# Kernel tuning notes

Hardware: AMD Instinct MI355X
Metric: run time of the kernel (lower is better)

The kernel has to match this reference:

```python
import jax, jax.numpy as jnp
import numpy as np

N_NODES = 50000
N_EDGES = 800000
IN_DIM = 162
HID = 256  # layer_1_feats == layer_2_feats (required by the stack op)


def _lin(k, fan_in, fan_out):
    kw, kb = jax.random.split(k)
    bound = 1.0 / np.sqrt(fan_in)
    w = jax.random.uniform(kw, (fan_in, fan_out), jnp.float32, -bound, bound)
    b = jax.random.uniform(kb, (fan_out,), jnp.float32, -bound, bound)
    return w, b


def setup_inputs() -> dict:
    key = jax.random.key(0)
    ks = jax.random.split(key, 12)
    feat = jax.random.normal(ks[0], (N_NODES, IN_DIM), jnp.float32)
    edge_index = jax.random.randint(ks[1], (2, N_EDGES), 0, N_NODES, jnp.int64)
    g0_w, g0_b = _lin(ks[2], IN_DIM, HID)
    g1_w, g1_b = _lin(ks[3], HID, HID)
    g2_w, g2_b = _lin(ks[4], HID, HID)
    gl_w, gl_b = _lin(ks[5], HID, HID)
    m1a_w, m1a_b = _lin(ks[6], IN_DIM, HID)
    m1b_w, m1b_b = _lin(ks[7], HID, HID)
    m2a_w, m2a_b = _lin(ks[8], HID, HID)
    m2b_w, m2b_b = _lin(ks[9], HID, HID)
    return dict(feat=feat, edge_index=edge_index,
                g0_w=g0_w, g0_b=g0_b, g1_w=g1_w, g1_b=g1_b,
                g2_w=g2_w, g2_b=g2_b, gl_w=gl_w, gl_b=gl_b,
                m1a_w=m1a_w, m1a_b=m1a_b, m1b_w=m1b_w, m1b_b=m1b_b,
                m2a_w=m2a_w, m2a_b=m2a_b, m2b_w=m2b_w, m2b_b=m2b_b)


def _gin_conv(x, src, dst, wa, ba, wb, bb):
    # DGL GINConv('sum'), eps=0: h = MLP(x + sum_{u->v} x[u])
    agg = jax.ops.segment_sum(x[src], dst, num_segments=N_NODES)
    h = jax.nn.relu((x + agg) @ wa + ba)
    return jax.nn.relu(h @ wb + bb)


def reference(feat, edge_index, g0_w, g0_b, g1_w, g1_b, g2_w, g2_b,
              gl_w, gl_b, m1a_w, m1a_b, m1b_w, m1b_b, m2a_w, m2a_b,
              m2b_w, m2b_b):
    src, dst = edge_index[0], edge_index[1]
    # layer-0 graph embedding from raw features
    g_emb0 = jax.nn.relu(jnp.sum(feat, 0) @ g0_w + g0_b)
    # GIN layer 1
    node1 = _gin_conv(feat, src, dst, m1a_w, m1a_b, m1b_w, m1b_b)
    g_emb1 = jax.nn.relu(jnp.sum(node1, 0) @ g1_w + g1_b)
    # GIN layer 2
    node2 = _gin_conv(node1, src, dst, m2a_w, m2a_b, m2b_w, m2b_b)
    g_emb2 = jax.nn.relu(jnp.sum(node2, 0) @ g2_w + g2_b)
    # sum of per-layer graph embeddings -> last linear
    g_sum = g_emb0 + g_emb1 + g_emb2
    g_last = jax.nn.relu(g_sum @ gl_w + gl_b)
    return node2 + g_last  # broadcast [N, HID] + [HID]
```

## Files before the change

kernel.cpp:

```cpp
#include <hip/hip_runtime.h>

#define N_NODES 50000
#define N_EDGES 800000
#define IN_DIM  162
#define HID     256
#define KPAD1   192
#define NB      ((N_NODES + 255) / 256)

typedef __bf16 bf16;
typedef __bf16 bf16x8 __attribute__((ext_vector_type(8)));
typedef __bf16 bf16x4 __attribute__((ext_vector_type(4)));
typedef float  f32x4  __attribute__((ext_vector_type(4)));
typedef float  f32x8  __attribute__((ext_vector_type(8)));
typedef float  f32x16 __attribute__((ext_vector_type(16)));

__device__ __forceinline__ void wf_one(const float* W, bf16* Wf, int K, int E)
{
    int e    = E & 7;
    int lane = (E >> 3) & 63;
    int fb   = (E >> 9) & 15;
    int ks   = E >> 13;
    int n = (fb >> 1) * 32 + (lane & 31);
    int k = ks * 32 + (fb & 1) * 16 + (lane >> 5) * 8 + e;
    Wf[E] = (k < K) ? (bf16)W[(size_t)k * HID + n] : (bf16)0.0f;
}

__global__ void wt_fragmajor_all(const float* __restrict__ m1aw, const float* __restrict__ m1bw,
                                 const float* __restrict__ m2aw, const float* __restrict__ m2bw,
                                 bf16* __restrict__ Wf1, bf16* __restrict__ Wf2,
                                 bf16* __restrict__ Wf3, bf16* __restrict__ Wf4)
{
    const int R1 = HID * KPAD1;
    const int R2 = HID * HID;
    int idx = blockIdx.x * blockDim.x + threadIdx.x;
    if (idx < R1)                 wf_one(m1aw, Wf1, IN_DIM, idx);
    else if (idx < R1 + R2)       wf_one(m1bw, Wf2, HID, idx - R1);
    else if (idx < R1 + 2 * R2)   wf_one(m2aw, Wf3, HID, idx - R1 - R2);
    else if (idx < R1 + 3 * R2)   wf_one(m2bw, Wf4, HID, idx - R1 - 2 * R2);
}

__global__ void feat_to_bf16(const float* __restrict__ feat, bf16* __restrict__ featbf)
{
    int idx = blockIdx.x * blockDim.x + threadIdx.x;
    int r = idx / (KPAD1 / 4);
    int c4 = (idx - r * (KPAD1 / 4)) * 4;
    if (r >= N_NODES) return;
    bf16x4 o;
#pragma unroll
    for (int j = 0; j < 4; ++j) {
        int c = c4 + j;
        o[j] = (c < IN_DIM) ? (bf16)feat[(size_t)r * IN_DIM + c] : (bf16)0.0f;
    }
    int gch = c4 / 24;
    int off = c4 - gch * 24;
    *(bf16x4*)(featbf + ((size_t)gch * N_NODES + r) * 24 + off) = o;
}

__global__ void colsum_feat8(const float* __restrict__ feat, float* __restrict__ colsum8)
{
    int c  = threadIdx.x;
    int r0 = blockIdx.x * 50;
    if (c >= IN_DIM) return;
    float acc = 0.0f;
#pragma unroll 2
    for (int i = 0; i < 50; ++i) {
        int r = r0 + i;
        if (r < N_NODES) acc += feat[(size_t)r * IN_DIM + c];
    }
    atomicAdd(&colsum8[(blockIdx.x & 7) * KPAD1 + c], acc);
}

__global__ void degree_hist(const int* __restrict__ dst, int* __restrict__ deg)
{
    int e = blockIdx.x * blockDim.x + threadIdx.x;
    atomicAdd(&deg[dst[e]], 1);
}

__global__ void block_degsum(const int* __restrict__ deg, int* __restrict__ bsum)
{
    __shared__ int s[256];
    int t = threadIdx.x;
    int idx = blockIdx.x * 256 + t;
    int v = (idx < N_NODES) ? deg[idx] : 0;
    s[t] = v;
    __syncthreads();
    for (int off = 128; off > 0; off >>= 1) {
        if (t < off) s[t] += s[t + off];
        __syncthreads();
    }
    if (t == 0) bsum[blockIdx.x] = s[0];
}

__global__ void scan_bsum(const int* __restrict__ bsum, int* __restrict__ gsum)
{
    __shared__ int s[256];
    int t = threadIdx.x;
    int v = (t < NB) ? bsum[t] : 0;
    s[t] = v;
    __syncthreads();
    for (int off = 1; off < 256; off <<= 1) {
        int u = (t >= off) ? s[t - off] : 0;
        __syncthreads();
        s[t] += u;
        __syncthreads();
    }
    gsum[t] = s[t] - v;
}

__global__ void block_scan_write(const int* __restrict__ deg, const int* __restrict__ gsum,
                                 int* __restrict__ rowptr, int* __restrict__ cursor)
{
    __shared__ int s[256];
    int t = threadIdx.x;
    int idx = blockIdx.x * 256 + t;
    int v = (idx < N_NODES) ? deg[idx] : 0;
    s[t] = v;
    __syncthreads();
    for (int off = 1; off < 256; off <<= 1) {
        int u = (t >= off) ? s[t - off] : 0;
        __syncthreads();
        s[t] += u;
        __syncthreads();
    }
    int excl = s[t] - v + gsum[blockIdx.x];
    if (idx < N_NODES) {
        rowptr[idx] = excl;
        cursor[idx] = excl;
    }
    if (idx == 0) rowptr[N_NODES] = N_EDGES;
}

__global__ void csr_fill(const int* __restrict__ src, const int* __restrict__ dst,
                         int* __restrict__ cursor, int* __restrict__ csr_src)
{
    int e = blockIdx.x * blockDim.x + threadIdx.x;
    int p = atomicAdd(&cursor[dst[e]], 1);
    csr_src[p] = src[e];
}

template<int CHUNK, int NACT>
__launch_bounds__(256)
__global__ void gather_v5(const bf16* __restrict__ xin,
                          const int* __restrict__ rowptr,
                          const int* __restrict__ csr_src,
                          bf16* __restrict__ xout)
{
    const int g    = blockIdx.x & 7;
    const int tile = blockIdx.x >> 3;
    const int wv   = threadIdx.x >> 6;
    const int lane = threadIdx.x & 63;
    const int q    = lane >> 4;
    const int j    = lane & 15;
    const int e    = j >> 2;
    const int c4   = j & 3;
    const int n    = tile * 16 + wv * 4 + q;
    const bool valid = (n < N_NODES);
    const bool act   = (c4 < NACT);
    const int  ce    = c4 * 8;
    const bf16* base = xin + (size_t)g * N_NODES * CHUNK;

    int r0 = 0, deg = 0;
    if (valid) {
        r0  = rowptr[n];
        deg = rowptr[n + 1] - r0;
    }

    int a0 = r0 + j;        if (a0 > N_EDGES - 1) a0 = N_EDGES - 1;
    int a1 = r0 + 16 + j;   if (a1 > N_EDGES - 1) a1 = N_EDGES - 1;
    const int i0 = csr_src[a0];
    const int i1 = csr_src[a1];

    f32x8 acc;
#pragma unroll
    for (int t = 0; t < 8; ++t) acc[t] = 0.0f;
    if (valid && e == 0 && act) {
        bf16x8 t0 = *(const bf16x8*)(base + (size_t)n * CHUNK + ce);
#pragma unroll
        for (int t = 0; t < 8; ++t) acc[t] = (float)t0[t];
    }

    const int lb = lane & ~3;

    {
        const int s0 = __shfl(i0, lb + 0, 64);
        const int s1 = __shfl(i0, lb + 1, 64);
        const int s2 = __shfl(i0, lb + 2, 64);
        const int s3 = __shfl(i0, lb + 3, 64);
        const int p0 = 4 * e;
        if (act) {
            bf16x8 u0 = *(const bf16x8*)(base + (size_t)s0 * CHUNK + ce);
            bf16x8 u1 = *(const bf16x8*)(base + (size_t)s1 * CHUNK + ce);
            bf16x8 u2 = *(const bf16x8*)(base + (size_t)s2 * CHUNK + ce);
            bf16x8 u3 = *(const bf16x8*)(base + (size_t)s3 * CHUNK + ce);
            if (p0 + 0 < deg) {
#pragma unroll
                for (int t = 0; t < 8; ++t) acc[t] += (float)u0[t];
            }
            if (p0 + 1 < deg) {
#pragma unroll
                for (int t = 0; t < 8; ++t) acc[t] += (float)u1[t];
            }
            if (p0 + 2 < deg) {
#pragma unroll
                for (int t = 0; t < 8; ++t) acc[t] += (float)u2[t];
            }
            if (p0 + 3 < deg) {
#pragma unroll
                for (int t = 0; t < 8; ++t) acc[t] += (float)u3[t];
            }
        }
    }

    {
        const int s0 = __shfl(i1, lb + 0, 64);
        const int s1 = __shfl(i1, lb + 1, 64);
        const int s2 = __shfl(i1, lb + 2, 64);
        const int s3 = __shfl(i1, lb + 3, 64);
        const int p0 = 16 + 4 * e;
        if (act && p0 < deg) {
            bf16x8 u0 = *(const bf16x8*)(base + (size_t)s0 * CHUNK + ce);
            bf16x8 u1 = *(const bf16x8*)(base + (size_t)s1 * CHUNK + ce);
            bf16x8 u2 = *(const bf16x8*)(base + (size_t)s2 * CHUNK + ce);
            bf16x8 u3 = *(const bf16x8*)(base + (size_t)s3 * CHUNK + ce);
            {
#pragma unroll
                for (int t = 0; t < 8; ++t) acc[t] += (float)u0[t];
            }
            if (p0 + 1 < deg) {
#pragma unroll
                for (int t = 0; t < 8; ++t) acc[t] += (float)u1[t];
            }
            if (p0 + 2 < deg) {
#pragma unroll
                for (int t = 0; t < 8; ++t) acc[t] += (float)u2[t];
            }
            if (p0 + 3 < deg) {
#pragma unroll
                for (int t = 0; t < 8; ++t) acc[t] += (float)u3[t];
            }
        }
    }

    for (int p = 32 + e; p < deg; p += 4) {
        const int s = csr_src[r0 + p];
        if (act) {
            bf16x8 u = *(const bf16x8*)(base + (size_t)s * CHUNK + ce);
#pragma unroll
            for (int t = 0; t < 8; ++t) acc[t] += (float)u[t];
        }
    }

#pragma unroll
    for (int t = 0; t < 8; ++t) {
        acc[t] += __shfl_xor(acc[t], 4, 64);
        acc[t] += __shfl_xor(acc[t], 8, 64);
    }

    if (valid && e == 0 && act) {
        bf16x8 o;
#pragma unroll
        for (int t = 0; t < 8; ++t) o[t] = (bf16)acc[t];
        __builtin_nontemporal_store(o,
            (bf16x8*)(xout + ((size_t)g * N_NODES + n) * CHUNK + ce));
    }
}

template<int KPAD, int ACHUNK, int OCHUNK>
__launch_bounds__(512)
__global__ void gemm_mlp8(const bf16* __restrict__ X,
                          const bf16* __restrict__ Wf1,
                          const float* __restrict__ bias1,
                          const bf16* __restrict__ Wf2,
                          const float* __restrict__ bias2,
                          bf16* __restrict__ out_bf,
                          float* __restrict__ colsum,
                          int M)
{
    __shared__ __align__(128) bf16 sH[64 * HID];
    __shared__ float cs[HID];

    const int tid  = threadIdx.x;
    const int w    = tid >> 6;
    const int lane = tid & 63;
    const int p    = lane >> 5;
    const int cn   = lane & 31;
    const int rw   = w & 1;
    const int cw   = w >> 1;
    const int m_base = blockIdx.x * 64;

    int arow = m_base + rw * 32 + cn;
    if (arow >= M) arow = M - 1;

    f32x16 accA, accB;
#pragma unroll
    for (int r = 0; r < 16; ++r) { accA[r] = 0.0f; accB[r] = 0.0f; }

#pragma unroll
    for (int ks = 0; ks < KPAD / 32; ++ks) {
#pragma unroll
        for (int kk = 0; kk < 2; ++kk) {
            bf16x8 a;
            if constexpr (ACHUNK == 0) {
                a = *(const bf16x8*)(X + (size_t)arow * KPAD + ks * 32 + kk * 16 + p * 8);
            } else {
                const int e   = ks * 32 + kk * 16 + p * 8;
                const int gch = e / ACHUNK;
                const int off = e - gch * ACHUNK;
                a = *(const bf16x8*)(X + ((size_t)gch * N_NODES + arow) * ACHUNK + off);
            }
            const int jg0 = cw * 2;
            bf16x8 b0 = *(const bf16x8*)(Wf1 + (((ks * 16 + (jg0 + 0) * 2 + kk) * 64) + lane) * 8);
            bf16x8 b1 = *(const bf16x8*)(Wf1 + (((ks * 16 + (jg0 + 1) * 2 + kk) * 64) + lane) * 8);
            accA = __builtin_amdgcn_mfma_f32_32x32x16_bf16(a, b0, accA, 0, 0, 0);
            accB = __builtin_amdgcn_mfma_f32_32x32x16_bf16(a, b1, accB, 0, 0, 0);
        }
    }

    char* sHb = (char*)sH;
#pragma unroll
    for (int jj = 0; jj < 2; ++jj) {
        const int col = cw * 64 + jj * 32 + cn;
        const float bv = bias1[col];
#pragma unroll
        for (int r = 0; r < 16; ++r) {
            const int rowl = (r & 3) + 8 * (r >> 2) + 4 * p;
            const int rowf = rw * 32 + rowl;
            float v = (jj == 0 ? accA[r] : accB[r]) + bv;
            v = v > 0.0f ? v : 0.0f;
            int ba = rowf * (HID * 2) + col * 2;
            ba ^= (rowf & 31) << 4;
            *(bf16*)(sHb + ba) = (bf16)v;
        }
    }
    __syncthreads();

#pragma unroll
    for (int r = 0; r < 16; ++r) { accA[r] = 0.0f; accB[r] = 0.0f; }

    const int hrow = rw * 32 + cn;
    const int hswz = (hrow & 31) << 4;
#pragma unroll
    for (int ks = 0; ks < HID / 32; ++ks) {
#pragma unroll
        for (int kk = 0; kk < 2; ++kk) {
            const int kb = (ks * 32 + kk * 16 + p * 8) * 2;
            bf16x8 a = *(const bf16x8*)(sHb + ((hrow * (HID * 2) + kb) ^ hswz));
            const int jg0 = cw * 2;
            bf16x8 b0 = *(const bf16x8*)(Wf2 + (((ks * 16 + (jg0 + 0) * 2 + kk) * 64) + lane) * 8);
            bf16x8 b1 = *(const bf16x8*)(Wf2 + (((ks * 16 + (jg0 + 1) * 2 + kk) * 64) + lane) * 8);
            accA = __builtin_amdgcn_mfma_f32_32x32x16_bf16(a, b0, accA, 0, 0, 0);
            accB = __builtin_amdgcn_mfma_f32_32x32x16_bf16(a, b1, accB, 0, 0, 0);
        }
    }

    if (colsum) {
        if (tid < HID) cs[tid] = 0.0f;
        __syncthreads();
    }

#pragma unroll
    for (int jj = 0; jj < 2; ++jj) {
        const int jg  = cw * 2 + jj;
        const int col = jg * 32 + cn;
        const float bv = bias2[col];
        float part = 0.0f;
#pragma unroll
        for (int r = 0; r < 16; ++r) {
            int rl = (r & 3) + 8 * (r >> 2) + 4 * p;
            int mo = m_base + rw * 32 + rl;
            if (mo < M) {
                float v = (jj == 0 ? accA[r] : accB[r]) + bv;
                v = v > 0.0f ? v : 0.0f;
                if constexpr (OCHUNK == 0)
                    out_bf[(size_t)mo * HID + col] = (bf16)v;
                else
                    out_bf[((size_t)jg * N_NODES + mo) * OCHUNK + cn] = (bf16)v;
                part += v;
            }
        }
        if (colsum) {
            part += __shfl_xor(part, 32, 64);
            if (p == 0) atomicAdd(&cs[col], part);
        }
    }

    if (colsum) {
        __syncthreads();
        if (tid < HID) atomicAdd(&colsum[tid], cs[tid]);
    }
}

__global__ void graph_head(const float* __restrict__ cs0_8,
                           const float* __restrict__ cs1,
                           const float* __restrict__ cs2,
                           const float* __restrict__ g0w, const float* __restrict__ g0b,
                           const float* __restrict__ g1w, const float* __restrict__ g1b,
                           const float* __restrict__ g2w, const float* __restrict__ g2b,
                           const float* __restrict__ glw, const float* __restrict__ glb,
                           float* __restrict__ gvec)
{
    __shared__ float v0[IN_DIM], v1[HID], v2[HID], gs[HID];
    int t = threadIdx.x;
    if (t < IN_DIM) {
        float s = 0.0f;
#pragma unroll
        for (int i = 0; i < 8; ++i) s += cs0_8[i * KPAD1 + t];
        v0[t] = s;
    }
    v1[t] = cs1[t];
    v2[t] = cs2[t];
    __syncthreads();

    float a0 = 0.0f, a1 = 0.0f, a2 = 0.0f;
    for (int k = 0; k < IN_DIM; ++k) a0 += v0[k] * g0w[k * HID + t];
    for (int k = 0; k < HID; ++k) {
        a1 += v1[k] * g1w[k * HID + t];
        a2 += v2[k] * g2w[k * HID + t];
    }
    float e0 = fmaxf(a0 + g0b[t], 0.0f);
    float e1 = fmaxf(a1 + g1b[t], 0.0f);
    float e2 = fmaxf(a2 + g2b[t], 0.0f);
    gs[t] = e0 + e1 + e2;
    __syncthreads();

    float a3 = 0.0f;
    for (int k = 0; k < HID; ++k) a3 += gs[k] * glw[k * HID + t];
    gvec[t] = fmaxf(a3 + glb[t], 0.0f);
}

__global__ void final_add(const bf16* __restrict__ node2,
                          const float* __restrict__ gvec,
                          float* __restrict__ out)
{
    int idx = blockIdx.x * blockDim.x + threadIdx.x;
    size_t base = (size_t)idx * 4;
    int c = (int)(base & (HID - 1));
    bf16x4 v = *(const bf16x4*)(node2 + base);
    f32x4 g = *(const f32x4*)(gvec + c);
    f32x4 o;
#pragma unroll
    for (int j = 0; j < 4; ++j) o[j] = (float)v[j] + g[j];
    *(f32x4*)(out + base) = o;
}

extern "C" void kernel_launch(void* const* d_in, const int* in_sizes, int n_in,
                              void* d_out, int out_size, void* d_ws, size_t ws_size,
                              hipStream_t stream)
{
    const float* feat = (const float*)d_in[0];
    const int*   ei   = (const int*)d_in[1];
    const int*   src  = ei;
    const int*   dst  = ei + N_EDGES;
    const float* g0w = (const float*)d_in[2],  *g0b = (const float*)d_in[3];
    const float* g1w = (const float*)d_in[4],  *g1b = (const float*)d_in[5];
    const float* g2w = (const float*)d_in[6],  *g2b = (const float*)d_in[7];
    const float* glw = (const float*)d_in[8],  *glb = (const float*)d_in[9];
    const float* m1aw = (const float*)d_in[10], *m1ab = (const float*)d_in[11];
    const float* m1bw = (const float*)d_in[12], *m1bb = (const float*)d_in[13];
    const float* m2aw = (const float*)d_in[14], *m2ab = (const float*)d_in[15];
    const float* m2bw = (const float*)d_in[16], *m2bb = (const float*)d_in[17];
    float* out = (float*)d_out;

    char* ws = (char*)d_ws;
    size_t off = 0;
    auto alloc = [&](size_t bytes) -> void* {
        void* p = ws + off;
        off += (bytes + 255) & ~(size_t)255;
        return p;
    };
    bf16*  featbf = (bf16*)alloc((size_t)N_NODES * KPAD1 * 2);
    bf16*  xsum  = (bf16*) alloc((size_t)N_NODES * KPAD1 * 2);
    bf16*  y2    = (bf16*) alloc((size_t)N_NODES * HID * 2);
    bf16*  node2 = (bf16*) alloc((size_t)N_NODES * HID * 2);
    bf16*  node1 = (bf16*) alloc((size_t)N_NODES * HID * 2);
    bf16*  Wf1   = (bf16*) alloc((size_t)HID * KPAD1 * 2);
    bf16*  Wf2   = (bf16*) alloc((size_t)HID * HID * 2);
    bf16*  Wf3   = (bf16*) alloc((size_t)HID * HID * 2);
    bf16*  Wf4   = (bf16*) alloc((size_t)HID * HID * 2);
    int*   deg     = (int*)alloc((size_t)N_NODES * 4);
    int*   rowptr  = (int*)alloc((size_t)(N_NODES + 1) * 4);
    int*   cursor  = (int*)alloc((size_t)N_NODES * 4);
    int*   csr_src = (int*)alloc((size_t)N_EDGES * 4);
    int*   bsum    = (int*)alloc(256 * 4);
    int*   gsum    = (int*)alloc(256 * 4);
    float* csums   = (float*)alloc((8 * KPAD1 + 256 + 256 + 256) * 4);
    float* colsum0_8 = csums;
    float* colsum1   = csums + 8 * KPAD1;
    float* colsum2   = csums + 8 * KPAD1 + 256;
    float* gvec      = csums + 8 * KPAD1 + 512;

    hipMemsetAsync(csums, 0, (8 * KPAD1 + 512) * 4, stream);
    hipMemsetAsync(deg, 0, (size_t)N_NODES * 4, stream);

    wt_fragmajor_all<<<(HID * KPAD1 + 3 * HID * HID + 255) / 256, 256, 0, stream>>>(
        m1aw, m1bw, m2aw, m2bw, Wf1, Wf2, Wf3, Wf4);

    feat_to_bf16<<<((size_t)N_NODES * (KPAD1 / 4) + 255) / 256, 256, 0, stream>>>(feat, featbf);
    colsum_feat8<<<1000, 192, 0, stream>>>(feat, colsum0_8);

    degree_hist<<<N_EDGES / 256, 256, 0, stream>>>(dst, deg);
    block_degsum<<<NB, 256, 0, stream>>>(deg, bsum);
    scan_bsum<<<1, 256, 0, stream>>>(bsum, gsum);
    block_scan_write<<<NB, 256, 0, stream>>>(deg, gsum, rowptr, cursor);
    csr_fill<<<N_EDGES / 256, 256, 0, stream>>>(src, dst, cursor, csr_src);

    const int gtiles = (N_NODES + 15) / 16;
    gather_v5<24, 3><<<gtiles * 8, 256, 0, stream>>>(featbf, rowptr, csr_src, xsum);

    const int gblocks = (N_NODES + 63) / 64;
    gemm_mlp8<KPAD1, 24, 32><<<gblocks, 512, 0, stream>>>(
        xsum, Wf1, m1ab, Wf2, m1bb, node1, colsum1, N_NODES);
    gather_v5<32, 4><<<gtiles * 8, 256, 0, stream>>>(node1, rowptr, csr_src, y2);
    gemm_mlp8<HID, 32, 0><<<gblocks, 512, 0, stream>>>(
        y2, Wf3, m2ab, Wf4, m2bb, node2, colsum2, N_NODES);
    graph_head<<<1, 256, 0, stream>>>(colsum0_8, colsum1, colsum2,
                                      g0w, g0b, g1w, g1b, g2w, g2b, glw, glb, gvec);
    final_add<<<((size_t)N_NODES * HID / 4 + 255) / 256, 256, 0, stream>>>(node2, gvec, out);
    (void)in_sizes; (void)n_in; (void)out_size; (void)ws_size;
}
```

Measured before the change: 468.3 us.

## Fuse prep kernels into one launch and retile MLP GEMM to 4 waves

```diff
diff --git a/kernel.cpp b/kernel.cpp
--- a/kernel.cpp
+++ b/kernel.cpp
@@ -25,55 +25,66 @@
     Wf[E] = (k < K) ? (bf16)W[(size_t)k * HID + n] : (bf16)0.0f;
 }
 
-__global__ void wt_fragmajor_all(const float* __restrict__ m1aw, const float* __restrict__ m1bw,
-                                 const float* __restrict__ m2aw, const float* __restrict__ m2bw,
-                                 bf16* __restrict__ Wf1, bf16* __restrict__ Wf2,
-                                 bf16* __restrict__ Wf3, bf16* __restrict__ Wf4)
-{
-    const int R1 = HID * KPAD1;
-    const int R2 = HID * HID;
-    int idx = blockIdx.x * blockDim.x + threadIdx.x;
-    if (idx < R1)                 wf_one(m1aw, Wf1, IN_DIM, idx);
-    else if (idx < R1 + R2)       wf_one(m1bw, Wf2, HID, idx - R1);
-    else if (idx < R1 + 2 * R2)   wf_one(m2aw, Wf3, HID, idx - R1 - R2);
-    else if (idx < R1 + 3 * R2)   wf_one(m2bw, Wf4, HID, idx - R1 - 2 * R2);
-}
-
-__global__ void feat_to_bf16(const float* __restrict__ feat, bf16* __restrict__ featbf)
-{
-    int idx = blockIdx.x * blockDim.x + threadIdx.x;
-    int r = idx / (KPAD1 / 4);
-    int c4 = (idx - r * (KPAD1 / 4)) * 4;
-    if (r >= N_NODES) return;
-    bf16x4 o;
-#pragma unroll
-    for (int j = 0; j < 4; ++j) {
-        int c = c4 + j;
-        o[j] = (c < IN_DIM) ? (bf16)feat[(size_t)r * IN_DIM + c] : (bf16)0.0f;
-    }
-    int gch = c4 / 24;
-    int off = c4 - gch * 24;
-    *(bf16x4*)(featbf + ((size_t)gch * N_NODES + r) * 24 + off) = o;
-}
-
-__global__ void colsum_feat8(const float* __restrict__ feat, float* __restrict__ colsum8)
-{
-    int c  = threadIdx.x;
-    int r0 = blockIdx.x * 50;
-    if (c >= IN_DIM) return;
-    float acc = 0.0f;
+#define WTB  ((HID * KPAD1 + 3 * HID * HID + 255) / 256)
+#define FTB  (((size_t)N_NODES * (KPAD1 / 4) + 255) / 256)
+#define CSB  1000
+#define DGB  (N_EDGES / 256)
+
+__global__ void prep_all(const float* __restrict__ m1aw, const float* __restrict__ m1bw,
+                         const float* __restrict__ m2aw, const float* __restrict__ m2bw,
+                         bf16* __restrict__ Wf1, bf16* __restrict__ Wf2,
+                         bf16* __restrict__ Wf3, bf16* __restrict__ Wf4,
+                         const float* __restrict__ feat, bf16* __restrict__ featbf,
+                         float* __restrict__ colsum8,
+                         const int* __restrict__ dst, int* __restrict__ deg)
+{
+    const int b   = blockIdx.x;
+    const int tid = threadIdx.x;
+
+    if (b < WTB) {
+        const int R1 = HID * KPAD1;
+        const int R2 = HID * HID;
+        int idx = b * 256 + tid;
+        if (idx < R1)                 wf_one(m1aw, Wf1, IN_DIM, idx);
+        else if (idx < R1 + R2)       wf_one(m1bw, Wf2, HID, idx - R1);
+        else if (idx < R1 + 2 * R2)   wf_one(m2aw, Wf3, HID, idx - R1 - R2);
+        else if (idx < R1 + 3 * R2)   wf_one(m2bw, Wf4, HID, idx - R1 - 2 * R2);
+        return;
+    }
+    if (b < WTB + FTB) {
+        int idx = (b - WTB) * 256 + tid;
+        int r = idx / (KPAD1 / 4);
+        int c4 = (idx - r * (KPAD1 / 4)) * 4;
+        if (r >= N_NODES) return;
+        bf16x4 o;
+#pragma unroll
+        for (int j = 0; j < 4; ++j) {
+            int c = c4 + j;
+            o[j] = (c < IN_DIM) ? (bf16)feat[(size_t)r * IN_DIM + c] : (bf16)0.0f;
+        }
+        int gch = c4 / 24;
+        int off = c4 - gch * 24;
+        *(bf16x4*)(featbf + ((size_t)gch * N_NODES + r) * 24 + off) = o;
+        return;
+    }
+    if (b < WTB + FTB + CSB) {
+        int csb = b - WTB - FTB;
+        int c = tid;
+        int r0 = csb * 50;
+        if (c >= IN_DIM) return;
+        float acc = 0.0f;
 #pragma unroll 2
-    for (int i = 0; i < 50; ++i) {
-        int r = r0 + i;
-        if (r < N_NODES) acc += feat[(size_t)r * IN_DIM + c];
-    }
-    atomicAdd(&colsum8[(blockIdx.x & 7) * KPAD1 + c], acc);
-}
-
-__global__ void degree_hist(const int* __restrict__ dst, int* __restrict__ deg)
-{
-    int e = blockIdx.x * blockDim.x + threadIdx.x;
-    atomicAdd(&deg[dst[e]], 1);
+        for (int i = 0; i < 50; ++i) {
+            int r = r0 + i;
+            if (r < N_NODES) acc += feat[(size_t)r * IN_DIM + c];
+        }
+        atomicAdd(&colsum8[(csb & 7) * KPAD1 + c], acc);
+        return;
+    }
+    {
+        int e = (b - WTB - FTB - CSB) * 256 + tid;
+        atomicAdd(&deg[dst[e]], 1);
+    }
 }
 
 __global__ void block_degsum(const int* __restrict__ deg, int* __restrict__ bsum)
@@ -266,8 +277,8 @@
 }
 
 template<int KPAD, int ACHUNK, int OCHUNK>
-__launch_bounds__(512)
-__global__ void gemm_mlp8(const bf16* __restrict__ X,
+__launch_bounds__(256)
+__global__ void gemm_mlp4(const bf16* __restrict__ X,
                           const bf16* __restrict__ Wf1,
                           const float* __restrict__ bias1,
                           const bf16* __restrict__ Wf2,
@@ -284,72 +295,100 @@
     const int lane = tid & 63;
     const int p    = lane >> 5;
     const int cn   = lane & 31;
-    const int rw   = w & 1;
-    const int cw   = w >> 1;
     const int m_base = blockIdx.x * 64;
-
-    int arow = m_base + rw * 32 + cn;
-    if (arow >= M) arow = M - 1;
-
-    f32x16 accA, accB;
-#pragma unroll
-    for (int r = 0; r < 16; ++r) { accA[r] = 0.0f; accB[r] = 0.0f; }
-
-#pragma unroll
-    for (int ks = 0; ks < KPAD / 32; ++ks) {
-#pragma unroll
-        for (int kk = 0; kk < 2; ++kk) {
-            bf16x8 a;
-            if constexpr (ACHUNK == 0) {
-                a = *(const bf16x8*)(X + (size_t)arow * KPAD + ks * 32 + kk * 16 + p * 8);
-            } else {
-                const int e   = ks * 32 + kk * 16 + p * 8;
-                const int gch = e / ACHUNK;
-                const int off = e - gch * ACHUNK;
-                a = *(const bf16x8*)(X + ((size_t)gch * N_NODES + arow) * ACHUNK + off);
-            }
-            const int jg0 = cw * 2;
-            bf16x8 b0 = *(const bf16x8*)(Wf1 + (((ks * 16 + (jg0 + 0) * 2 + kk) * 64) + lane) * 8);
-            bf16x8 b1 = *(const bf16x8*)(Wf1 + (((ks * 16 + (jg0 + 1) * 2 + kk) * 64) + lane) * 8);
-            accA = __builtin_amdgcn_mfma_f32_32x32x16_bf16(a, b0, accA, 0, 0, 0);
-            accB = __builtin_amdgcn_mfma_f32_32x32x16_bf16(a, b1, accB, 0, 0, 0);
+    const int jg0  = w * 2;
+
+    int ar0 = m_base + cn;        if (ar0 >= M) ar0 = M - 1;
+    int ar1 = m_base + 32 + cn;   if (ar1 >= M) ar1 = M - 1;
+
+    f32x16 acc00, acc01, acc10, acc11;
+#pragma unroll
+    for (int r = 0; r < 16; ++r) { acc00[r] = 0.0f; acc01[r] = 0.0f; acc10[r] = 0.0f; acc11[r] = 0.0f; }
+
+    auto aptr = [&](int row, int t) -> const bf16* {
+        const int e = t * 16 + p * 8;
+        if constexpr (ACHUNK == 0) {
+            return X + (size_t)row * KPAD + e;
+        } else {
+            const int gch = e / ACHUNK;
+            const int off = e - gch * ACHUNK;
+            return X + ((size_t)gch * N_NODES + row) * ACHUNK + off;
+        }
+    };
+    auto bptr = [&](const bf16* Wf, int jg, int t) -> const bf16* {
+        const int ks = t >> 1, kk = t & 1;
+        return Wf + (((ks * 16 + jg * 2 + kk) * 64) + lane) * 8;
+    };
+
+    constexpr int T1 = KPAD / 16;
+    {
+        bf16x8 a0 = *(const bf16x8*)aptr(ar0, 0);
+        bf16x8 a1 = *(const bf16x8*)aptr(ar1, 0);
+        bf16x8 b0 = *(const bf16x8*)bptr(Wf1, jg0, 0);
+        bf16x8 b1 = *(const bf16x8*)bptr(Wf1, jg0 + 1, 0);
+#pragma unroll
+        for (int t = 0; t < T1; ++t) {
+            bf16x8 na0 = a0, na1 = a1, nb0 = b0, nb1 = b1;
+            if (t + 1 < T1) {
+                na0 = *(const bf16x8*)aptr(ar0, t + 1);
+                na1 = *(const bf16x8*)aptr(ar1, t + 1);
+                nb0 = *(const bf16x8*)bptr(Wf1, jg0, t + 1);
+                nb1 = *(const bf16x8*)bptr(Wf1, jg0 + 1, t + 1);
+            }
+            acc00 = __builtin_amdgcn_mfma_f32_32x32x16_bf16(a0, b0, acc00, 0, 0, 0);
+            acc01 = __builtin_amdgcn_mfma_f32_32x32x16_bf16(a0, b1, acc01, 0, 0, 0);
+            acc10 = __builtin_amdgcn_mfma_f32_32x32x16_bf16(a1, b0, acc10, 0, 0, 0);
+            acc11 = __builtin_amdgcn_mfma_f32_32x32x16_bf16(a1, b1, acc11, 0, 0, 0);
+            a0 = na0; a1 = na1; b0 = nb0; b1 = nb1;
         }
     }
 
     char* sHb = (char*)sH;
 #pragma unroll
-    for (int jj = 0; jj < 2; ++jj) {
-        const int col = cw * 64 + jj * 32 + cn;
-        const float bv = bias1[col];
-#pragma unroll
-        for (int r = 0; r < 16; ++r) {
-            const int rowl = (r & 3) + 8 * (r >> 2) + 4 * p;
-            const int rowf = rw * 32 + rowl;
-            float v = (jj == 0 ? accA[r] : accB[r]) + bv;
-            v = v > 0.0f ? v : 0.0f;
-            int ba = rowf * (HID * 2) + col * 2;
-            ba ^= (rowf & 31) << 4;
-            *(bf16*)(sHb + ba) = (bf16)v;
+    for (int rh = 0; rh < 2; ++rh) {
+#pragma unroll
+        for (int jj = 0; jj < 2; ++jj) {
+            const int col = w * 64 + jj * 32 + cn;
+            const float bv = bias1[col];
+#pragma unroll
+            for (int r = 0; r < 16; ++r) {
+                const int rowl = (r & 3) + 8 * (r >> 2) + 4 * p;
+                const int rowf = rh * 32 + rowl;
+                float v = (rh == 0 ? (jj == 0 ? acc00[r] : acc01[r])
+                                   : (jj == 0 ? acc10[r] : acc11[r])) + bv;
+                v = v > 0.0f ? v : 0.0f;
+                int ba = rowf * (HID * 2) + col * 2;
+                ba ^= (rowf & 31) << 4;
+                *(bf16*)(sHb + ba) = (bf16)v;
+            }
         }
     }
     __syncthreads();
 
 #pragma unroll
-    for (int r = 0; r < 16; ++r) { accA[r] = 0.0f; accB[r] = 0.0f; }
-
-    const int hrow = rw * 32 + cn;
-    const int hswz = (hrow & 31) << 4;
-#pragma unroll
-    for (int ks = 0; ks < HID / 32; ++ks) {
-#pragma unroll
-        for (int kk = 0; kk < 2; ++kk) {
-            const int kb = (ks * 32 + kk * 16 + p * 8) * 2;
-            bf16x8 a = *(const bf16x8*)(sHb + ((hrow * (HID * 2) + kb) ^ hswz));
-            const int jg0 = cw * 2;
-            bf16x8 b0 = *(const bf16x8*)(Wf2 + (((ks * 16 + (jg0 + 0) * 2 + kk) * 64) + lane) * 8);
-            bf16x8 b1 = *(const bf16x8*)(Wf2 + (((ks * 16 + (jg0 + 1) * 2 + kk) * 64) + lane) * 8);
-            accA = __builtin_amdgcn_mfma_f32_32x32x16_bf16(a, b0, accA, 0, 0, 0);
-            accB = __builtin_amdgcn_mfma_f32_32x32x16_bf16(a, b1, accB, 0, 0, 0);
+    for (int r = 0; r < 16; ++r) { acc00[r] = 0.0f; acc01[r] = 0.0f; acc10[r] = 0.0f; acc11[r] = 0.0f; }
+
+    const int hr0 = cn, hr1 = 32 + cn;
+    const int hs0 = (hr0 & 31) << 4, hs1 = (hr1 & 31) << 4;
+    constexpr int T2 = HID / 16;
+    {
+        bf16x8 b0 = *(const bf16x8*)bptr(Wf2, jg0, 0);
+        bf16x8 b1 = *(const bf16x8*)bptr(Wf2, jg0 + 1, 0);
+#pragma unroll
+        for (int t = 0; t < T2; ++t) {
+            bf16x8 nb0 = b0, nb1 = b1;
+            if (t + 1 < T2) {
+                nb0 = *(const bf16x8*)bptr(Wf2, jg0, t + 1);
+                nb1 = *(const bf16x8*)bptr(Wf2, jg0 + 1, t + 1);
+            }
+            const int kb = (t * 16 + p * 8) * 2;
+            bf16x8 a0 = *(const bf16x8*)(sHb + ((hr0 * (HID * 2) + kb) ^ hs0));
+            bf16x8 a1 = *(const bf16x8*)(sHb + ((hr1 * (HID * 2) + kb) ^ hs1));
+            acc00 = __builtin_amdgcn_mfma_f32_32x32x16_bf16(a0, b0, acc00, 0, 0, 0);
+            acc01 = __builtin_amdgcn_mfma_f32_32x32x16_bf16(a0, b1, acc01, 0, 0, 0);
+            acc10 = __builtin_amdgcn_mfma_f32_32x32x16_bf16(a1, b0, acc10, 0, 0, 0);
+            acc11 = __builtin_amdgcn_mfma_f32_32x32x16_bf16(a1, b1, acc11, 0, 0, 0);
+            b0 = nb0; b1 = nb1;
         }
     }
 
@@ -360,22 +399,26 @@
 
 #pragma unroll
     for (int jj = 0; jj < 2; ++jj) {
-        const int jg  = cw * 2 + jj;
+        const int jg  = jg0 + jj;
         const int col = jg * 32 + cn;
         const float bv = bias2[col];
         float part = 0.0f;
 #pragma unroll
-        for (int r = 0; r < 16; ++r) {
-            int rl = (r & 3) + 8 * (r >> 2) + 4 * p;
-            int mo = m_base + rw * 32 + rl;
-            if (mo < M) {
-                float v = (jj == 0 ? accA[r] : accB[r]) + bv;
-                v = v > 0.0f ? v : 0.0f;
-                if constexpr (OCHUNK == 0)
-                    out_bf[(size_t)mo * HID + col] = (bf16)v;
-                else
-                    out_bf[((size_t)jg * N_NODES + mo) * OCHUNK + cn] = (bf16)v;
-                part += v;
+        for (int rh = 0; rh < 2; ++rh) {
+#pragma unroll
+            for (int r = 0; r < 16; ++r) {
+                int rl = rh * 32 + (r & 3) + 8 * (r >> 2) + 4 * p;
+                int mo = m_base + rl;
+                if (mo < M) {
+                    float v = (rh == 0 ? (jj == 0 ? acc00[r] : acc01[r])
+                                       : (jj == 0 ? acc10[r] : acc11[r])) + bv;
+                    v = v > 0.0f ? v : 0.0f;
+                    if constexpr (OCHUNK == 0)
+                        out_bf[(size_t)mo * HID + col] = (bf16)v;
+                    else
+                        out_bf[((size_t)jg * N_NODES + mo) * OCHUNK + cn] = (bf16)v;
+                    part += v;
+                }
             }
         }
         if (colsum) {
@@ -492,13 +535,10 @@
     hipMemsetAsync(csums, 0, (8 * KPAD1 + 512) * 4, stream);
     hipMemsetAsync(deg, 0, (size_t)N_NODES * 4, stream);
 
-    wt_fragmajor_all<<<(HID * KPAD1 + 3 * HID * HID + 255) / 256, 256, 0, stream>>>(
-        m1aw, m1bw, m2aw, m2bw, Wf1, Wf2, Wf3, Wf4);
-
-    feat_to_bf16<<<((size_t)N_NODES * (KPAD1 / 4) + 255) / 256, 256, 0, stream>>>(feat, featbf);
-    colsum_feat8<<<1000, 192, 0, stream>>>(feat, colsum0_8);
-
-    degree_hist<<<N_EDGES / 256, 256, 0, stream>>>(dst, deg);
+    prep_all<<<WTB + FTB + CSB + DGB, 256, 0, stream>>>(
+        m1aw, m1bw, m2aw, m2bw, Wf1, Wf2, Wf3, Wf4,
+        feat, featbf, colsum0_8, dst, deg);
+
     block_degsum<<<NB, 256, 0, stream>>>(deg, bsum);
     scan_bsum<<<1, 256, 0, stream>>>(bsum, gsum);
     block_scan_write<<<NB, 256, 0, stream>>>(deg, gsum, rowptr, cursor);
@@ -508,10 +548,10 @@
     gather_v5<24, 3><<<gtiles * 8, 256, 0, stream>>>(featbf, rowptr, csr_src, xsum);
 
     const int gblocks = (N_NODES + 63) / 64;
-    gemm_mlp8<KPAD1, 24, 32><<<gblocks, 512, 0, stream>>>(
+    gemm_mlp4<KPAD1, 24, 32><<<gblocks, 256, 0, stream>>>(
         xsum, Wf1, m1ab, Wf2, m1bb, node1, colsum1, N_NODES);
     gather_v5<32, 4><<<gtiles * 8, 256, 0, stream>>>(node1, rowptr, csr_src, y2);
-    gemm_mlp8<HID, 32, 0><<<gblocks, 512, 0, stream>>>(
+    gemm_mlp4<HID, 32, 0><<<gblocks, 256, 0, stream>>>(
         y2, Wf3, m2ab, Wf4, m2bb, node2, colsum2, N_NODES);
     graph_head<<<1, 256, 0, stream>>>(colsum0_8, colsum1, colsum2,
                                       g0w, g0b, g1w, g1b, g2w, g2b, glw, glb, gvec);
```

Measured after the change: 465.8 us. About the same (-0.5%).
